# Performance work log

Hardware: AMD Instinct MI355X
Metric: run time of the kernel (lower is better)

## Reference

```python
import jax, jax.numpy as jnp
import numpy as np

EPS = 1e-4
HEADS = 8
DIM_HEAD = 32
BALANCE = 0.3


def _normalize(x, dims):
    # torch normalize(): norm over `dims` in fp32; norm = eps + norm*sqrt(norm.numel()/x.numel())
    red = 1
    for d in dims:
        red *= x.shape[d]
    norm = jnp.sqrt(jnp.sum(jnp.square(x.astype(jnp.float32)), axis=dims, keepdims=True))
    norm = EPS + norm / np.sqrt(red)
    return x / norm.astype(x.dtype)


def _mpconv1x1(x, w, gain=1.0):
    # MPConv forward (eval mode): weight-normalize per output channel, scale, 1x1 conv
    w = w.astype(jnp.float32)
    w = _normalize(w, (1, 2, 3))
    fan_in = w.shape[1] * w.shape[2] * w.shape[3]
    w = (w * (gain / np.sqrt(fan_in))).astype(x.dtype)[:, :, 0, 0]  # [out, in]
    return jnp.einsum('oi,nihw->nohw', w, x)


def setup_inputs() -> dict:
    key = jax.random.key(0)
    k1, k2, k3 = jax.random.split(key, 3)
    x = jax.random.normal(k1, (2, 256, 48, 48), dtype=jnp.float32)
    w_qkv = jax.random.normal(k2, (768, 256, 1, 1), dtype=jnp.float32)
    w_out = jax.random.normal(k3, (256, 256, 1, 1), dtype=jnp.float32)
    return {"x": x, "w_qkv": w_qkv, "w_out": w_out}


def reference(x, w_qkv, w_out):
    n, c, h, w_sp = x.shape
    seq = h * w_sp
    y = _mpconv1x1(x, w_qkv)                          # [n, 3c, h, w]
    y = y.reshape(n, HEADS, DIM_HEAD, 3, seq)         # channel split: head x dim_head x 3
    y = _normalize(y, (2,))                           # L2-normalize over dim_head axis
    q = y[:, :, :, 0, :]
    k = y[:, :, :, 1, :]
    v = y[:, :, :, 2, :]
    # scores [n, h, q, k] with k scaled by 1/sqrt(dim_head)
    att = jax.nn.softmax(jnp.einsum('nhcq,nhck->nhqk', q, k) / np.sqrt(DIM_HEAD), axis=3)
    y = jnp.einsum('nhqk,nhck->nhcq', att, v)         # [n, heads, dim_head, seq]
    y = _mpconv1x1(y.reshape(n, c, h, w_sp), w_out)
    t = BALANCE
    # mp_sum: lerp then magnitude-preserving rescale
    return (x + t * (y - x)) / np.sqrt((1 - t) ** 2 + t ** 2)
```

## Files before the change

### kernel.cpp

```cpp
#include <hip/hip_runtime.h>
#include <math.h>

#define EPSN 1e-4f
#define SEQ 2304

using bf16x8 = __attribute__((ext_vector_type(8))) short;
using f32x4  = __attribute__((ext_vector_type(4))) float;

__device__ inline unsigned short f2bf(float x) {
    union { float f; unsigned u; } c; c.f = x;
    unsigned u = c.u;
    u += 0x7fffu + ((u >> 16) & 1u);
    return (unsigned short)(u >> 16);
}

__global__ __launch_bounds__(256) void prep_kernel(const float* __restrict__ w_qkv,
                                                   const float* __restrict__ w_out,
                                                   const float* __restrict__ x,
                                                   unsigned short* __restrict__ wqb,
                                                   unsigned short* __restrict__ wob,
                                                   unsigned short* __restrict__ xt) {
    __shared__ __align__(16) unsigned short T[64][80];
    __shared__ float red[4];
    __shared__ float scale_s;
    int bid = blockIdx.x;
    if (bid < 1024) {
        const float* src;
        unsigned short* dst;
        if (bid < 768) { src = w_qkv + bid * 256; dst = wqb + bid * 256; }
        else           { src = w_out + (bid - 768) * 256; dst = wob + (bid - 768) * 256; }
        float v = src[threadIdx.x];
        float ss = v * v;
        for (int off = 32; off > 0; off >>= 1) ss += __shfl_down(ss, off, 64);
        int lane = threadIdx.x & 63, wid = threadIdx.x >> 6;
        if (lane == 0) red[wid] = ss;
        __syncthreads();
        if (threadIdx.x == 0) {
            float t = red[0] + red[1] + red[2] + red[3];
            scale_s = 1.0f / (sqrtf(t) + 16.0f * EPSN);
        }
        __syncthreads();
        dst[threadIdx.x] = f2bf(v * scale_s);
    } else {
        int e0 = bid - 1024;
        int st = e0 % 36, ct = (e0 / 36) & 3, n = e0 / 144;
        int t = threadIdx.x;
#pragma unroll
        for (int p = 0; p < 4; ++p) {
            int e = t + p * 256;
            int c = e >> 4, sv = (e & 15) * 4;
            float4 v = *(const float4*)&x[(size_t)(n * 256 + ct * 64 + c) * SEQ + st * 64 + sv];
            T[sv + 0][c] = f2bf(v.x);
            T[sv + 1][c] = f2bf(v.y);
            T[sv + 2][c] = f2bf(v.z);
            T[sv + 3][c] = f2bf(v.w);
        }
        __syncthreads();
#pragma unroll
        for (int p = 0; p < 2; ++p) {
            int e = t + p * 256;
            int s = e >> 3, cb = (e & 7) * 8;
            uint4 v = *(const uint4*)&T[s][cb];
            *(uint4*)&xt[(size_t)(n * SEQ + st * 64 + s) * 256 + ct * 64 + cb] = v;
        }
    }
}

__global__ __launch_bounds__(256) void qkv_fused_kernel(const unsigned short* __restrict__ xt,
                                                        const unsigned short* __restrict__ wqb,
                                                        unsigned short* __restrict__ qn,
                                                        unsigned short* __restrict__ kn,
                                                        unsigned short* __restrict__ vn) {
    __shared__ __align__(16) char smem[96 * 65 * 4];
    float (*Cs)[65] = (float(*)[65])smem;
    int h  = blockIdx.x;
    int st = blockIdx.y;
    int n  = blockIdx.z;
    int tid = threadIdx.x;
    int wave = tid >> 6, lane = tid & 63;
    int ln = lane & 15, quad = lane >> 4;
    const unsigned short* Abase = wqb + (size_t)(h * 96 + ln) * 256 + quad * 8;
    const unsigned short* Bbase = xt + (size_t)(n * SEQ + st * 64 + wave * 16 + ln) * 256 + quad * 8;
    f32x4 acc[6];
#pragma unroll
    for (int m = 0; m < 6; ++m) acc[m] = (f32x4){0.f, 0.f, 0.f, 0.f};
#pragma unroll
    for (int kc = 0; kc < 8; ++kc) {
        bf16x8 b = *(const bf16x8*)(Bbase + kc * 32);
#pragma unroll
        for (int m = 0; m < 6; ++m) {
            bf16x8 a = *(const bf16x8*)(Abase + (size_t)(m * 16) * 256 + kc * 32);
            acc[m] = __builtin_amdgcn_mfma_f32_16x16x32_bf16(a, b, acc[m], 0, 0, 0);
        }
    }
#pragma unroll
    for (int m = 0; m < 6; ++m)
#pragma unroll
        for (int r = 0; r < 4; ++r)
            Cs[m * 16 + quad * 4 + r][wave * 16 + ln] = acc[m][r];
    __syncthreads();
    int sl = tid & 63, wh = tid >> 6;
    float v[32];
    float inv = 0.f;
    if (tid < 192) {
        float ss = 0.f;
#pragma unroll
        for (int d = 0; d < 32; ++d) { v[d] = Cs[3 * d + wh][sl]; ss += v[d] * v[d]; }
        inv = 1.0f / (EPSN + sqrtf(ss * (1.0f / 32.0f)));
        if (wh == 0) inv *= 0.2550348660352446f;
    }
    __syncthreads();
    unsigned short (*Sq)[40] = (unsigned short(*)[40])smem;
    unsigned short (*Sk)[40] = (unsigned short(*)[40])(smem + 5120);
    unsigned short (*Sv)[72] = (unsigned short(*)[72])(smem + 10240);
    if (tid < 192) {
        if (wh == 2) {
#pragma unroll
            for (int d = 0; d < 32; ++d) Sv[d][sl] = f2bf(v[d] * inv);
        } else {
            unsigned short (*S)[40] = wh ? Sk : Sq;
#pragma unroll
            for (int j = 0; j < 16; ++j) {
                unsigned p = (unsigned)f2bf(v[2 * j] * inv) | ((unsigned)f2bf(v[2 * j + 1] * inv) << 16);
                *(unsigned*)&S[sl][2 * j] = p;
            }
        }
    }
    __syncthreads();
    int nh = n * 8 + h;
    size_t qkbase = (size_t)nh * 73728 + (size_t)st * 2048;
    {
        int s = tid >> 2, d8 = (tid & 3) * 8;
        uint4 t4 = *(uint4*)&Sq[s][d8];
        *(uint4*)(qn + qkbase + tid * 8) = t4;
        uint4 k4 = *(uint4*)&Sk[s][d8];
        *(uint4*)(kn + qkbase + tid * 8) = k4;
        int dv = tid >> 3, s8 = (tid & 7) * 8;
        uint4 v4 = *(uint4*)&Sv[dv][s8];
        *(uint4*)(vn + (size_t)nh * 73728 + (size_t)dv * SEQ + st * 64 + s8) = v4;
    }
}

__global__ __launch_bounds__(256) void attn_mfma_kernel(const unsigned short* __restrict__ qn,
                                                        const unsigned short* __restrict__ kn,
                                                        const unsigned short* __restrict__ vn,
                                                        float* __restrict__ Opart,
                                                        float* __restrict__ Lpart) {
    __shared__ __align__(16) unsigned short Ks[2][64][40];
    __shared__ __align__(16) unsigned short Vs[2][32][72];
    __shared__ __align__(16) unsigned short Ps[4][16][72];
    int tid = threadIdx.x;
    int wave = tid >> 6, lane = tid & 63;
    int ln = lane & 15, quad = lane >> 4;
    int qt = blockIdx.x, nh = blockIdx.y, kz = blockIdx.z;
    const unsigned short* Qg = qn + (size_t)nh * 73728;
    const unsigned short* Kg = kn + (size_t)nh * 73728;
    const unsigned short* Vg = vn + (size_t)nh * 73728;

    bf16x8 qf = *(const bf16x8*)(Qg + (size_t)(qt * 64 + wave * 16 + ln) * 32 + quad * 8);
    bf16x8 ones;
#pragma unroll
    for (int i = 0; i < 8; ++i) ones[i] = (short)0x3F80;

    f32x4 o0 = {0.f, 0.f, 0.f, 0.f};
    f32x4 o1 = {0.f, 0.f, 0.f, 0.f};
    f32x4 lac = {0.f, 0.f, 0.f, 0.f};

    int kt0 = kz * 12;
    uint4 kreg = *(const uint4*)(Kg + (size_t)(kt0 * 64) * 32 + tid * 8);
    uint4 vreg = *(const uint4*)(Vg + (size_t)(tid >> 3) * SEQ + kt0 * 64 + (tid & 7) * 8);
    *(uint4*)(&Ks[0][tid >> 2][(tid & 3) * 8]) = kreg;
    *(uint4*)(&Vs[0][tid >> 3][(tid & 7) * 8]) = vreg;

    for (int i = 0; i < 12; ++i) {
        int buf = i & 1;
        if (i + 1 < 12) {
            int k0n = (kt0 + i + 1) * 64;
            kreg = *(const uint4*)(Kg + (size_t)k0n * 32 + tid * 8);
            vreg = *(const uint4*)(Vg + (size_t)(tid >> 3) * SEQ + k0n + (tid & 7) * 8);
        }
        __syncthreads();

        const f32x4 zero = {0.f, 0.f, 0.f, 0.f};
#pragma unroll
        for (int c = 0; c < 4; ++c) {
            bf16x8 kf = *(const bf16x8*)(&Ks[buf][c * 16 + ln][quad * 8]);
            f32x4 sc = __builtin_amdgcn_mfma_f32_16x16x32_bf16(qf, kf, zero, 0, 0, 0);
#pragma unroll
            for (int r = 0; r < 4; ++r) {
                unsigned u = __float_as_uint(exp2f(sc[r]));
                Ps[wave][quad * 4 + r][c * 16 + ln] = (unsigned short)(u >> 16);
            }
        }
#pragma unroll
        for (int kc = 0; kc < 2; ++kc) {
            bf16x8 pf = *(const bf16x8*)(&Ps[wave][ln][kc * 32 + quad * 8]);
            bf16x8 v0 = *(const bf16x8*)(&Vs[buf][ln][kc * 32 + quad * 8]);
            bf16x8 v1 = *(const bf16x8*)(&Vs[buf][16 + ln][kc * 32 + quad * 8]);
            lac = __builtin_amdgcn_mfma_f32_16x16x32_bf16(pf, ones, lac, 0, 0, 0);
            o0  = __builtin_amdgcn_mfma_f32_16x16x32_bf16(pf, v0, o0, 0, 0, 0);
            o1  = __builtin_amdgcn_mfma_f32_16x16x32_bf16(pf, v1, o1, 0, 0, 0);
        }
        if (i + 1 < 12) {
            *(uint4*)(&Ks[buf ^ 1][tid >> 2][(tid & 3) * 8]) = kreg;
            *(uint4*)(&Vs[buf ^ 1][tid >> 3][(tid & 7) * 8]) = vreg;
        }
    }

    float* Ob = Opart + ((size_t)(kz * 16 + nh) * 36 + qt) * 2048;
    float* Lb = Lpart + ((size_t)(kz * 16 + nh) * 36 + qt) * 64;
#pragma unroll
    for (int r = 0; r < 4; ++r) {
        int ql = wave * 16 + quad * 4 + r;
        Ob[ql * 32 + ln]      = o0[r];
        Ob[ql * 32 + 16 + ln] = o1[r];
        if (ln == 0) Lb[ql] = lac[r];
    }
}

__global__ __launch_bounds__(256) void attn_reduce_kernel(const float* __restrict__ Opart,
                                                          const float* __restrict__ Lpart,
                                                          unsigned short* __restrict__ y2t) {
    int qt = blockIdx.x, nh = blockIdx.y;
    int n = nh >> 3, h = nh & 7;
    size_t s0 = (size_t)nh * 36 + qt;
    const float* O0 = Opart + s0 * 2048;
    const float* O1 = Opart + (s0 + 36 * 16) * 2048;
    const float* O2 = Opart + (s0 + 72 * 16) * 2048;
    const float* L0 = Lpart + s0 * 64;
    const float* L1 = Lpart + (s0 + 36 * 16) * 64;
    const float* L2 = Lpart + (s0 + 72 * 16) * 64;
#pragma unroll
    for (int p = 0; p < 8; ++p) {
        int idx = threadIdx.x + p * 256;
        int q = idx >> 5, c = idx & 31;
        float l = L0[q] + L1[q] + L2[q];
        float v = (O0[idx] + O1[idx] + O2[idx]) / l;
        y2t[((size_t)(n * SEQ) + qt * 64 + q) * 256 + h * 32 + c] = f2bf(v);
    }
}

__global__ __launch_bounds__(256) void out_gemm_kernel(const unsigned short* __restrict__ y2t,
                                                       const unsigned short* __restrict__ wob,
                                                       const float* __restrict__ x,
                                                       float* __restrict__ out) {
    int mt = blockIdx.x;
    int st = blockIdx.y;
    int n  = blockIdx.z;
    int tid = threadIdx.x;
    int wave = tid >> 6, lane = tid & 63;
    int ln = lane & 15, quad = lane >> 4;
    int m0 = mt * 64 + wave * 16;
    const unsigned short* Abase = wob + (size_t)(m0 + ln) * 256 + quad * 8;
    const unsigned short* Bbase = y2t + (size_t)(n * SEQ + st * 64 + ln) * 256 + quad * 8;
    f32x4 acc[4];
#pragma unroll
    for (int c = 0; c < 4; ++c) acc[c] = (f32x4){0.f, 0.f, 0.f, 0.f};
#pragma unroll
    for (int kc = 0; kc < 8; ++kc) {
        bf16x8 a = *(const bf16x8*)(Abase + kc * 32);
#pragma unroll
        for (int c = 0; c < 4; ++c) {
            bf16x8 b = *(const bf16x8*)(Bbase + (size_t)(c * 16) * 256 + kc * 32);
            acc[c] = __builtin_amdgcn_mfma_f32_16x16x32_bf16(a, b, acc[c], 0, 0, 0);
        }
    }
    const float c0f = 0.7f * 1.3130643285972254f;
    const float c1f = 0.3f * 1.3130643285972254f;
#pragma unroll
    for (int c = 0; c < 4; ++c)
#pragma unroll
        for (int r = 0; r < 4; ++r) {
            int o = m0 + quad * 4 + r;
            int s = st * 64 + c * 16 + ln;
            size_t idx = (size_t)(n * 256 + o) * SEQ + s;
            out[idx] = c0f * x[idx] + c1f * acc[c][r];
        }
}

extern "C" void kernel_launch(void* const* d_in, const int* in_sizes, int n_in,
                              void* d_out, int out_size, void* d_ws, size_t ws_size,
                              hipStream_t stream) {
    (void)in_sizes; (void)n_in; (void)out_size; (void)ws_size;
    const float* x     = (const float*)d_in[0];
    const float* w_qkv = (const float*)d_in[1];
    const float* w_out = (const float*)d_in[2];
    float* out = (float*)d_out;
    float* ws  = (float*)d_ws;
    unsigned short* wqb = (unsigned short*)(ws);
    unsigned short* wob = (unsigned short*)(ws + 98304);
    unsigned short* xt  = (unsigned short*)(ws + 131072);
    unsigned short* y2t = (unsigned short*)(ws + 131072);
    unsigned short* qn  = (unsigned short*)(ws + 720896);
    unsigned short* kn  = (unsigned short*)(ws + 1310720);
    unsigned short* vn  = (unsigned short*)(ws + 1900544);
    float* Opart = ws + 2490368;
    float* Lpart = ws + 6029312;

    hipLaunchKernelGGL(prep_kernel, dim3(1312), dim3(256), 0, stream,
                       w_qkv, w_out, x, wqb, wob, xt);
    hipLaunchKernelGGL(qkv_fused_kernel, dim3(8, 36, 2), dim3(256), 0, stream,
                       xt, wqb, qn, kn, vn);
    hipLaunchKernelGGL(attn_mfma_kernel, dim3(36, 16, 3), dim3(256), 0, stream,
                       qn, kn, vn, Opart, Lpart);
    hipLaunchKernelGGL(attn_reduce_kernel, dim3(36, 16), dim3(256), 0, stream,
                       Opart, Lpart, y2t);
    hipLaunchKernelGGL(out_gemm_kernel, dim3(4, 36, 2), dim3(256), 0, stream,
                       y2t, wob, x, out);
}
```

Before: 133.2 us.

## Process two query tiles per wave and split keys four ways in attention

Each wave now handles 32 query rows instead of 16, reusing the K and V fragments it loads from shared memory across both query sub-tiles. The split-K factor changes from 3 to 4 with 9 key tiles per block, and the partial-output layout is flattened so the reduce kernel sums four partials. The score MFMA operands are swapped so the P tile can be written to shared memory as packed 64-bit stores instead of scalar shorts. This lowers LDS traffic per FLOP but uses more registers and adds partial-sum traffic through the larger Opart buffer.

```diff
diff --git a/kernel.cpp b/kernel.cpp
--- a/kernel.cpp
+++ b/kernel.cpp
@@ -152,69 +152,96 @@
     int tid = threadIdx.x;
     int wave = tid >> 6, lane = tid & 63;
     int ln = lane & 15, quad = lane >> 4;
-    int qt = blockIdx.x, nh = blockIdx.y, kz = blockIdx.z;
+    int qp = blockIdx.x, nh = blockIdx.y, kz = blockIdx.z;
     const unsigned short* Qg = qn + (size_t)nh * 73728;
     const unsigned short* Kg = kn + (size_t)nh * 73728;
     const unsigned short* Vg = vn + (size_t)nh * 73728;
-
-    bf16x8 qf = *(const bf16x8*)(Qg + (size_t)(qt * 64 + wave * 16 + ln) * 32 + quad * 8);
+    int qbase = qp * 128 + wave * 32;
+
+    bf16x8 qf0 = *(const bf16x8*)(Qg + (size_t)(qbase + ln) * 32 + quad * 8);
+    bf16x8 qf1 = *(const bf16x8*)(Qg + (size_t)(qbase + 16 + ln) * 32 + quad * 8);
     bf16x8 ones;
 #pragma unroll
     for (int i = 0; i < 8; ++i) ones[i] = (short)0x3F80;
 
-    f32x4 o0 = {0.f, 0.f, 0.f, 0.f};
-    f32x4 o1 = {0.f, 0.f, 0.f, 0.f};
-    f32x4 lac = {0.f, 0.f, 0.f, 0.f};
-
-    int kt0 = kz * 12;
+    f32x4 o00 = {0.f,0.f,0.f,0.f}, o01 = {0.f,0.f,0.f,0.f};
+    f32x4 o10 = {0.f,0.f,0.f,0.f}, o11 = {0.f,0.f,0.f,0.f};
+    f32x4 lac0 = {0.f,0.f,0.f,0.f}, lac1 = {0.f,0.f,0.f,0.f};
+    const f32x4 zero = {0.f,0.f,0.f,0.f};
+
+    const int NIT = 9;
+    int kt0 = kz * NIT;
     uint4 kreg = *(const uint4*)(Kg + (size_t)(kt0 * 64) * 32 + tid * 8);
     uint4 vreg = *(const uint4*)(Vg + (size_t)(tid >> 3) * SEQ + kt0 * 64 + (tid & 7) * 8);
     *(uint4*)(&Ks[0][tid >> 2][(tid & 3) * 8]) = kreg;
     *(uint4*)(&Vs[0][tid >> 3][(tid & 7) * 8]) = vreg;
 
-    for (int i = 0; i < 12; ++i) {
+    for (int i = 0; i < NIT; ++i) {
         int buf = i & 1;
-        if (i + 1 < 12) {
+        if (i + 1 < NIT) {
             int k0n = (kt0 + i + 1) * 64;
             kreg = *(const uint4*)(Kg + (size_t)k0n * 32 + tid * 8);
             vreg = *(const uint4*)(Vg + (size_t)(tid >> 3) * SEQ + k0n + (tid & 7) * 8);
         }
         __syncthreads();
 
-        const f32x4 zero = {0.f, 0.f, 0.f, 0.f};
-#pragma unroll
-        for (int c = 0; c < 4; ++c) {
-            bf16x8 kf = *(const bf16x8*)(&Ks[buf][c * 16 + ln][quad * 8]);
-            f32x4 sc = __builtin_amdgcn_mfma_f32_16x16x32_bf16(qf, kf, zero, 0, 0, 0);
-#pragma unroll
-            for (int r = 0; r < 4; ++r) {
-                unsigned u = __float_as_uint(exp2f(sc[r]));
-                Ps[wave][quad * 4 + r][c * 16 + ln] = (unsigned short)(u >> 16);
+        bf16x8 kf[4];
+#pragma unroll
+        for (int c = 0; c < 4; ++c)
+            kf[c] = *(const bf16x8*)(&Ks[buf][c * 16 + ln][quad * 8]);
+        bf16x8 vfa[2], vfb[2];
+#pragma unroll
+        for (int kc = 0; kc < 2; ++kc) {
+            vfa[kc] = *(const bf16x8*)(&Vs[buf][ln][kc * 32 + quad * 8]);
+            vfb[kc] = *(const bf16x8*)(&Vs[buf][16 + ln][kc * 32 + quad * 8]);
+        }
+#pragma unroll
+        for (int t = 0; t < 2; ++t) {
+            bf16x8 qf = t ? qf1 : qf0;
+#pragma unroll
+            for (int c = 0; c < 4; ++c) {
+                f32x4 sc = __builtin_amdgcn_mfma_f32_16x16x32_bf16(kf[c], qf, zero, 0, 0, 0);
+                unsigned e0 = __float_as_uint(exp2f(sc[0]));
+                unsigned e1 = __float_as_uint(exp2f(sc[1]));
+                unsigned e2 = __float_as_uint(exp2f(sc[2]));
+                unsigned e3 = __float_as_uint(exp2f(sc[3]));
+                unsigned p01 = (e0 >> 16) | (e1 & 0xffff0000u);
+                unsigned p23 = (e2 >> 16) | (e3 & 0xffff0000u);
+                *(uint2*)&Ps[wave][ln][c * 16 + quad * 4] = make_uint2(p01, p23);
             }
-        }
-#pragma unroll
-        for (int kc = 0; kc < 2; ++kc) {
-            bf16x8 pf = *(const bf16x8*)(&Ps[wave][ln][kc * 32 + quad * 8]);
-            bf16x8 v0 = *(const bf16x8*)(&Vs[buf][ln][kc * 32 + quad * 8]);
-            bf16x8 v1 = *(const bf16x8*)(&Vs[buf][16 + ln][kc * 32 + quad * 8]);
-            lac = __builtin_amdgcn_mfma_f32_16x16x32_bf16(pf, ones, lac, 0, 0, 0);
-            o0  = __builtin_amdgcn_mfma_f32_16x16x32_bf16(pf, v0, o0, 0, 0, 0);
-            o1  = __builtin_amdgcn_mfma_f32_16x16x32_bf16(pf, v1, o1, 0, 0, 0);
-        }
-        if (i + 1 < 12) {
+#pragma unroll
+            for (int kc = 0; kc < 2; ++kc) {
+                bf16x8 pf = *(const bf16x8*)(&Ps[wave][ln][kc * 32 + quad * 8]);
+                if (t == 0) {
+                    lac0 = __builtin_amdgcn_mfma_f32_16x16x32_bf16(pf, ones, lac0, 0, 0, 0);
+                    o00  = __builtin_amdgcn_mfma_f32_16x16x32_bf16(pf, vfa[kc], o00, 0, 0, 0);
+                    o01  = __builtin_amdgcn_mfma_f32_16x16x32_bf16(pf, vfb[kc], o01, 0, 0, 0);
+                } else {
+                    lac1 = __builtin_amdgcn_mfma_f32_16x16x32_bf16(pf, ones, lac1, 0, 0, 0);
+                    o10  = __builtin_amdgcn_mfma_f32_16x16x32_bf16(pf, vfa[kc], o10, 0, 0, 0);
+                    o11  = __builtin_amdgcn_mfma_f32_16x16x32_bf16(pf, vfb[kc], o11, 0, 0, 0);
+                }
+            }
+        }
+        if (i + 1 < NIT) {
             *(uint4*)(&Ks[buf ^ 1][tid >> 2][(tid & 3) * 8]) = kreg;
             *(uint4*)(&Vs[buf ^ 1][tid >> 3][(tid & 7) * 8]) = vreg;
         }
     }
 
-    float* Ob = Opart + ((size_t)(kz * 16 + nh) * 36 + qt) * 2048;
-    float* Lb = Lpart + ((size_t)(kz * 16 + nh) * 36 + qt) * 64;
+    size_t obase = (size_t)(kz * 16 + nh) * 2304;
 #pragma unroll
     for (int r = 0; r < 4; ++r) {
-        int ql = wave * 16 + quad * 4 + r;
-        Ob[ql * 32 + ln]      = o0[r];
-        Ob[ql * 32 + 16 + ln] = o1[r];
-        if (ln == 0) Lb[ql] = lac[r];
+        int q0 = qbase + quad * 4 + r;
+        Opart[(obase + q0) * 32 + ln]      = o00[r];
+        Opart[(obase + q0) * 32 + 16 + ln] = o01[r];
+        int q1 = q0 + 16;
+        Opart[(obase + q1) * 32 + ln]      = o10[r];
+        Opart[(obase + q1) * 32 + 16 + ln] = o11[r];
+        if (ln == 0) {
+            Lpart[obase + q0] = lac0[r];
+            Lpart[obase + q1] = lac1[r];
+        }
     }
 }
 
@@ -223,19 +250,15 @@
                                                           unsigned short* __restrict__ y2t) {
     int qt = blockIdx.x, nh = blockIdx.y;
     int n = nh >> 3, h = nh & 7;
-    size_t s0 = (size_t)nh * 36 + qt;
-    const float* O0 = Opart + s0 * 2048;
-    const float* O1 = Opart + (s0 + 36 * 16) * 2048;
-    const float* O2 = Opart + (s0 + 72 * 16) * 2048;
-    const float* L0 = Lpart + s0 * 64;
-    const float* L1 = Lpart + (s0 + 36 * 16) * 64;
-    const float* L2 = Lpart + (s0 + 72 * 16) * 64;
+    size_t base = (size_t)nh * 2304 + qt * 64;
+    const size_t KZS = (size_t)16 * 2304;
 #pragma unroll
     for (int p = 0; p < 8; ++p) {
         int idx = threadIdx.x + p * 256;
         int q = idx >> 5, c = idx & 31;
-        float l = L0[q] + L1[q] + L2[q];
-        float v = (O0[idx] + O1[idx] + O2[idx]) / l;
+        float l = Lpart[base + q] + Lpart[base + KZS + q] + Lpart[base + 2 * KZS + q] + Lpart[base + 3 * KZS + q];
+        size_t ob = (base + q) * 32 + c;
+        float v = (Opart[ob] + Opart[ob + KZS * 32] + Opart[ob + 2 * KZS * 32] + Opart[ob + 3 * KZS * 32]) / l;
         y2t[((size_t)(n * SEQ) + qt * 64 + q) * 256 + h * 32 + c] = f2bf(v);
     }
 }
@@ -295,13 +318,13 @@
     unsigned short* kn  = (unsigned short*)(ws + 1310720);
     unsigned short* vn  = (unsigned short*)(ws + 1900544);
     float* Opart = ws + 2490368;
-    float* Lpart = ws + 6029312;
+    float* Lpart = ws + 7208960;
 
     hipLaunchKernelGGL(prep_kernel, dim3(1312), dim3(256), 0, stream,
                        w_qkv, w_out, x, wqb, wob, xt);
     hipLaunchKernelGGL(qkv_fused_kernel, dim3(8, 36, 2), dim3(256), 0, stream,
                        xt, wqb, qn, kn, vn);
-    hipLaunchKernelGGL(attn_mfma_kernel, dim3(36, 16, 3), dim3(256), 0, stream,
+    hipLaunchKernelGGL(attn_mfma_kernel, dim3(18, 16, 4), dim3(256), 0, stream,
                        qn, kn, vn, Opart, Lpart);
     hipLaunchKernelGGL(attn_reduce_kernel, dim3(36, 16), dim3(256), 0, stream,
                        Opart, Lpart, y2t);
```

Result: no change. 134.4 us (+0.9%).
